# Optimization experiments

Measured on AMD Instinct MI355X. Metric: run time of the kernel, lower is better.

Reference implementation:

```python
import jax, jax.numpy as jnp
import numpy as np

TGT_LEN = 1024
MEM_LEN = 1024
SAME_LENGTH = True
D_MODEL = 2048
BATCH = 4


def _make_ft_real(tgt_len: int, mem_len: int, same_length: bool) -> jnp.ndarray:
    """Build the banded Fourier mixing matrix. Since the module's input x is real
    and only .real of the output is returned, Re(FT @ x) == Re(FT) @ x, so we
    precompute only the real part (this also matches the kernel-headroom note:
    the imaginary output is never used)."""
    qlen = tgt_len
    klen = tgt_len + mem_len
    flen = klen - qlen + 1
    m = np.outer(np.arange(qlen), np.arange(flen))
    ft = np.exp(2j * np.pi * m / flen) / np.sqrt(flen)  # [qlen, flen] complex
    ft = np.pad(ft, ((0, 0), (klen - flen, 0)))          # left-pad to [qlen, klen]
    for i in range(qlen):  # setup-time numpy loop over fixed qlen rows (not traced)
        ft[i] = np.roll(ft[i], -(qlen - i - 1))
    ft = np.tril(ft, klen - qlen)
    if same_length:
        ft = np.triu(ft, 0)
    return jnp.asarray(ft.real.astype(np.float32))


_FT_REAL = _make_ft_real(TGT_LEN, MEM_LEN, SAME_LENGTH)  # [tgt_len, tgt_len+mem_len]


def setup_inputs() -> dict:
    key = jax.random.key(0)
    k1, k2 = jax.random.split(key)
    klen = TGT_LEN + MEM_LEN
    x = jax.random.normal(k1, (BATCH, klen, D_MODEL), dtype=jnp.float32)
    p = jax.random.normal(k2, (BATCH, klen, D_MODEL), dtype=jnp.float32)
    return {"x": x, "p": p, "qlen": TGT_LEN, "add_position": 1}


def reference(x, p, qlen, add_position):
    # Dropout is identity in eval mode (deterministic reference).
    if add_position:
        x = x + p
    klen = x.shape[1]
    ft = _FT_REAL[-qlen:, -klen:]                    # [qlen, klen]
    scale = np.float32(1.0 / np.sqrt(klen))
    # Banded token-mixing matmul; real part only (x is real).
    out = jnp.einsum("lm,bmd->bld", ft, x) * scale   # [B, qlen, D]
    return out
```

## Files before the change

kernel.cpp:

```cpp
#include <hip/hip_runtime.h>
#include <hip/hip_bf16.h>
#include <cstdint>

#define QLEN   1024
#define KLEN   2048
#define DMODEL 2048
#define BATCH  4
#define FLEN   (KLEN - QLEN + 1)

typedef __bf16 bf16x8 __attribute__((ext_vector_type(8)));
typedef float  f32x4  __attribute__((ext_vector_type(4)));

__device__ __align__(16) __bf16 g_ft[(size_t)QLEN * KLEN];
__device__ __align__(16) __bf16 g_yt[(size_t)BATCH * DMODEL * KLEN];

typedef __attribute__((address_space(1))) void gvoid;
typedef __attribute__((address_space(3))) void svoid;

__device__ __forceinline__ void async_load16(const void* g, void* lds) {
  gvoid* gp = (gvoid*)(uintptr_t)g;
  svoid* sp = (svoid*)(uint32_t)(uintptr_t)lds;
  __builtin_amdgcn_global_load_lds(gp, sp, 16, 0, 0);
}

#define YT_UNITS (BATCH * (KLEN / 8) * (DMODEL / 64))
#define FT_UNITS ((QLEN * KLEN) / 512)

__global__ __launch_bounds__(256) void prep_kernel(const float* __restrict__ x,
                                                   const float* __restrict__ p,
                                                   const int* __restrict__ addp,
                                                   __bf16* __restrict__ ftp,
                                                   __bf16* __restrict__ ytp) {
  __bf16* ft = ftp ? ftp : g_ft;
  __bf16* yt = ytp ? ytp : g_yt;
  const int lane  = threadIdx.x & 63;
  const int gw    = (blockIdx.x * 256 + threadIdx.x) >> 6;
  const int nw    = gridDim.x * 4;
  const int doadd = *addp;

  for (int u = gw; u < YT_UNITS + FT_UNITS; u += nw) {
    if (u < YT_UNITS) {
      const int b  = u >> 13;
      const int r5 = u & 8191;
      const int mt = r5 >> 5;
      const int db = r5 & 31;
      const int d  = db * 64 + lane;
      const float* xp = x + ((size_t)b * KLEN + mt * 8) * DMODEL + d;
      float v[8];
#pragma unroll
      for (int i = 0; i < 8; ++i) v[i] = xp[(size_t)i * DMODEL];
      if (doadd) {
        const float* pp = p + ((size_t)b * KLEN + mt * 8) * DMODEL + d;
#pragma unroll
        for (int i = 0; i < 8; ++i) v[i] += pp[(size_t)i * DMODEL];
      }
      bf16x8 o;
#pragma unroll
      for (int i = 0; i < 8; ++i) o[i] = (__bf16)v[i];
      *(bf16x8*)(yt + ((size_t)b * (KLEN / 8) * DMODEL + (size_t)mt * DMODEL + d) * 8) = o;
    } else {
      const int uu = (u - YT_UNITS) * 64 + lane;
      const int l  = uu >> 8;
      const int m0 = (uu & 255) * 8;
      const int j0 = m0 - l;
      bf16x8 o = {};
      if (j0 + 7 >= 0 && j0 < FLEN) {
        const float w     = 6.283185307179586f / (float)FLEN;
        const float scale = 1.0f / sqrtf((float)FLEN * (float)KLEN);
#pragma unroll
        for (int i = 0; i < 8; ++i) {
          const int j = j0 + i;
          float vv = 0.0f;
          if (j >= 0 && j < FLEN) {
            const int rr = (l * j) % FLEN;
            vv = cosf((float)rr * w) * scale;
          }
          o[i] = (__bf16)vv;
        }
      }
      *(bf16x8*)(ft + (size_t)uu * 8) = o;
    }
  }
}

#define BM 128
#define BN 128
#define BK 64

__global__ __launch_bounds__(256) void gemm_kernel(float* __restrict__ out,
                                                   const __bf16* __restrict__ ftq,
                                                   const __bf16* __restrict__ ytq) {
  __shared__ __align__(16) __bf16 As[BM * BK];
  __shared__ __align__(16) __bf16 Bs[BN * BK];
  const int bn = blockIdx.x, bm = blockIdx.y, b = blockIdx.z;
  const int l0 = bm * BM, d0 = bn * BN;
  const int tid  = threadIdx.x;
  const int lane = tid & 63;
  const int wave = tid >> 6;
  const int wr = wave >> 1, wc = wave & 1;
  const int col = lane & 15, quad = lane >> 4;

  f32x4 acc[4][4] = {};

  const int t0 = l0 >> 6;
  const int t1 = (l0 + BM - 1 + FLEN - 1) >> 6;
  const __bf16* ftp = ftq ? ftq : g_ft;
  const __bf16* ytp = (ytq ? ytq : g_yt) + (size_t)b * DMODEL * KLEN;

  for (int t = t0; t <= t1; ++t) {
    const int k0 = t * BK;
#pragma unroll
    for (int s = 0; s < 4; ++s) {
      const int cb  = wave * 256 + s * 64;
      const int lc  = cb + lane;
      const int row = lc >> 3;
      const int gc8 = (lc & 7) ^ (row & 7);
      async_load16(ftp + (size_t)(l0 + row) * KLEN + k0 + gc8 * 8, As + cb * 8);
    }
#pragma unroll
    for (int s = 0; s < 4; ++s) {
      const int idx = wave * 256 + s * 64 + lane;
      const int c   = idx >> 7;
      const int dd  = idx & 127;
      async_load16(ytp + ((size_t)(t * 8 + c) * DMODEL + (d0 + dd)) * 8, Bs + (size_t)idx * 8);
    }
    __syncthreads();

#pragma unroll
    for (int kk = 0; kk < 2; ++kk) {
      bf16x8 af[4], bq[4];
      const int c8 = kk * 4 + quad;
#pragma unroll
      for (int ti = 0; ti < 4; ++ti) {
        const int r = wr * 64 + ti * 16 + col;
        af[ti] = *(const bf16x8*)(As + (size_t)((r << 3) + (c8 ^ (r & 7))) * 8);
      }
#pragma unroll
      for (int tj = 0; tj < 4; ++tj) {
        const int r = wc * 64 + tj * 16 + col;
        bq[tj] = *(const bf16x8*)(Bs + (size_t)((c8 << 7) + r) * 8);
      }
#pragma unroll
      for (int ti = 0; ti < 4; ++ti)
#pragma unroll
        for (int tj = 0; tj < 4; ++tj)
          acc[ti][tj] = __builtin_amdgcn_mfma_f32_16x16x32_bf16(af[ti], bq[tj], acc[ti][tj], 0, 0, 0);
    }
    __syncthreads();
  }

#pragma unroll
  for (int ti = 0; ti < 4; ++ti) {
    const int l = l0 + wr * 64 + ti * 16 + quad * 4;
#pragma unroll
    for (int tj = 0; tj < 4; ++tj) {
      const int d = d0 + wc * 64 + tj * 16 + col;
      float* op = out + (size_t)b * QLEN * DMODEL + (size_t)l * DMODEL + d;
#pragma unroll
      for (int r2 = 0; r2 < 4; ++r2) op[(size_t)r2 * DMODEL] = acc[ti][tj][r2];
    }
  }
}

extern "C" void kernel_launch(void* const* d_in, const int* in_sizes, int n_in,
                              void* d_out, int out_size, void* d_ws, size_t ws_size,
                              hipStream_t stream) {
  const float* x   = (const float*)d_in[0];
  const float* p   = (const float*)d_in[1];
  const int* addp  = (const int*)d_in[3];
  float* out = (float*)d_out;

  const size_t FT_BYTES = (size_t)QLEN * KLEN * sizeof(__bf16);
  const size_t YT_BYTES = (size_t)BATCH * DMODEL * KLEN * sizeof(__bf16);
  __bf16* ft = nullptr;
  __bf16* yt = nullptr;
  char* ws = (char*)d_ws;
  if (ws && ws_size >= FT_BYTES + YT_BYTES) {
    ft = (__bf16*)ws;
    yt = (__bf16*)(ws + FT_BYTES);
  } else if (ws && ws_size >= YT_BYTES) {
    yt = (__bf16*)ws;
  }

  prep_kernel<<<dim3(2048), dim3(256), 0, stream>>>(x, p, addp, ft, yt);
  gemm_kernel<<<dim3(DMODEL / BN, QLEN / BM, BATCH), dim3(256), 0, stream>>>(out, ft, yt);
}
```

Baseline: 188.7 us.

## Vectorize prep loads with float4 and permute yt layout to match

The prep kernel now reads x and p as 16-byte float4 vectors, four d-columns per lane, and issues all loads before converting. It writes the bf16 transposed buffer in a new permuted layout. The GEMM's B-tile address calculation is changed to match that layout, and the prep grid is halved. The goal is to cut the memory-bound prep cost from scalar 4-byte loads. The trade-offs are that p is now always loaded even when add_position is zero, and the GEMM B-tile reads are less contiguous.

Result: slower. 194.2 us (+2.9%).

```diff
diff --git a/kernel.cpp b/kernel.cpp
--- a/kernel.cpp
+++ b/kernel.cpp
@@ -23,8 +23,9 @@
   __builtin_amdgcn_global_load_lds(gp, sp, 16, 0, 0);
 }
 
-#define YT_UNITS (BATCH * (KLEN / 8) * (DMODEL / 64))
+#define YT_UNITS (BATCH * (KLEN / 8) * (DMODEL / 256))
 #define FT_UNITS ((QLEN * KLEN) / 512)
+#define PREP_BLOCKS 1024
 
 __global__ __launch_bounds__(256) void prep_kernel(const float* __restrict__ x,
                                                    const float* __restrict__ p,
@@ -36,28 +37,30 @@
   const int lane  = threadIdx.x & 63;
   const int gw    = (blockIdx.x * 256 + threadIdx.x) >> 6;
   const int nw    = gridDim.x * 4;
-  const int doadd = *addp;
+  const float addf = (*addp) ? 1.0f : 0.0f;
 
   for (int u = gw; u < YT_UNITS + FT_UNITS; u += nw) {
     if (u < YT_UNITS) {
-      const int b  = u >> 13;
-      const int r5 = u & 8191;
-      const int mt = r5 >> 5;
-      const int db = r5 & 31;
-      const int d  = db * 64 + lane;
-      const float* xp = x + ((size_t)b * KLEN + mt * 8) * DMODEL + d;
-      float v[8];
+      const int b  = u >> 11;
+      const int r  = u & 2047;
+      const int mt = r >> 3;
+      const int g  = r & 7;
+      const f32x4* xp4 = (const f32x4*)(x + ((size_t)b * KLEN + mt * 8) * DMODEL + g * 256 + 4 * lane);
+      const f32x4* pp4 = (const f32x4*)(p + ((size_t)b * KLEN + mt * 8) * DMODEL + g * 256 + 4 * lane);
+      f32x4 vx[8], vp[8];
 #pragma unroll
-      for (int i = 0; i < 8; ++i) v[i] = xp[(size_t)i * DMODEL];
-      if (doadd) {
-        const float* pp = p + ((size_t)b * KLEN + mt * 8) * DMODEL + d;
+      for (int i = 0; i < 8; ++i) vx[i] = xp4[(size_t)i * (DMODEL / 4)];
 #pragma unroll
-        for (int i = 0; i < 8; ++i) v[i] += pp[(size_t)i * DMODEL];
+      for (int i = 0; i < 8; ++i) vp[i] = pp4[(size_t)i * (DMODEL / 4)];
+      __builtin_amdgcn_sched_barrier(0);
+      __bf16* op = yt + (size_t)b * (size_t)(DMODEL * KLEN) + mt * 16384 + g * 2048 + lane * 8;
+#pragma unroll
+      for (int j = 0; j < 4; ++j) {
+        bf16x8 o;
+#pragma unroll
+        for (int i = 0; i < 8; ++i) o[i] = (__bf16)(vx[i][j] + addf * vp[i][j]);
+        *(bf16x8*)(op + j * 512) = o;
       }
-      bf16x8 o;
-#pragma unroll
-      for (int i = 0; i < 8; ++i) o[i] = (__bf16)v[i];
-      *(bf16x8*)(yt + ((size_t)b * (KLEN / 8) * DMODEL + (size_t)mt * DMODEL + d) * 8) = o;
     } else {
       const int uu = (u - YT_UNITS) * 64 + lane;
       const int l  = uu >> 8;
@@ -122,7 +125,10 @@
       const int idx = wave * 256 + s * 64 + lane;
       const int c   = idx >> 7;
       const int dd  = idx & 127;
-      async_load16(ytp + ((size_t)(t * 8 + c) * DMODEL + (d0 + dd)) * 8, Bs + (size_t)idx * 8);
+      const int mtg = t * 8 + c;
+      const size_t src = (size_t)mtg * 16384 + (bn >> 1) * 2048
+                       + (dd & 3) * 512 + (((bn & 1) << 5) + (dd >> 2)) * 8;
+      async_load16(ytp + src, Bs + (size_t)idx * 8);
     }
     __syncthreads();
 
@@ -182,6 +188,6 @@
     yt = (__bf16*)ws;
   }
 
-  prep_kernel<<<dim3(2048), dim3(256), 0, stream>>>(x, p, addp, ft, yt);
+  prep_kernel<<<dim3(PREP_BLOCKS), dim3(256), 0, stream>>>(x, p, addp, ft, yt);
   gemm_kernel<<<dim3(DMODEL / BN, QLEN / BM, BATCH), dim3(256), 0, stream>>>(out, ft, yt);
 }
```

## Fuse prep and GEMM into one kernel with per-batch flag dependencies

Applied to the files above, without the earlier changes.

Merges the conversion/FT-generation prep kernel and the banded GEMM into a single launch where prep blocks signal atomic counters and GEMM blocks spin-wait on the FT flag and their batch's flag. This lets GEMM work for early batches overlap with prep of later batches and removes the full inter-kernel barrier. It adds a tiny flag-reset kernel, spin-waits that depend on block dispatch order to avoid deadlock, and shares LDS allocation across all block roles.

New measurement: 389.2 us. 2.06x slower.

```diff
diff --git a/kernel.cpp b/kernel.cpp
--- a/kernel.cpp
+++ b/kernel.cpp
@@ -13,6 +13,7 @@
 
 __device__ __align__(16) __bf16 g_ft[(size_t)QLEN * KLEN];
 __device__ __align__(16) __bf16 g_yt[(size_t)BATCH * DMODEL * KLEN];
+__device__ int g_flags[8];
 
 typedef __attribute__((address_space(1))) void gvoid;
 typedef __attribute__((address_space(3))) void svoid;
@@ -23,50 +24,48 @@
   __builtin_amdgcn_global_load_lds(gp, sp, 16, 0, 0);
 }
 
-#define YT_UNITS (BATCH * (KLEN / 8) * (DMODEL / 64))
-#define FT_UNITS ((QLEN * KLEN) / 512)
-
-__global__ __launch_bounds__(256) void prep_kernel(const float* __restrict__ x,
-                                                   const float* __restrict__ p,
-                                                   const int* __restrict__ addp,
-                                                   __bf16* __restrict__ ftp,
-                                                   __bf16* __restrict__ ytp) {
+#define BM 128
+#define BN 128
+#define BK 64
+
+#define FT_BLOCKS  256
+#define YT_BLOCKS  (BATCH * 256)
+#define GEMM_PER_B 128
+#define GRID_TOTAL (FT_BLOCKS + YT_BLOCKS + BATCH * GEMM_PER_B)
+
+__global__ void init_flags_kernel(int* flagsp) {
+  int* flags = flagsp ? flagsp : g_flags;
+  if (threadIdx.x < 8) flags[threadIdx.x] = 0;
+}
+
+__global__ __launch_bounds__(256, 4) void fused_kernel(const float* __restrict__ x,
+                                                       const float* __restrict__ p,
+                                                       const int* __restrict__ addp,
+                                                       __bf16* __restrict__ ftp,
+                                                       __bf16* __restrict__ ytp,
+                                                       int* __restrict__ flagsp,
+                                                       float* __restrict__ out) {
+  __shared__ __align__(16) __bf16 As[BM * BK];
+  __shared__ __align__(16) __bf16 Bs[BN * BK];
   __bf16* ft = ftp ? ftp : g_ft;
   __bf16* yt = ytp ? ytp : g_yt;
-  const int lane  = threadIdx.x & 63;
-  const int gw    = (blockIdx.x * 256 + threadIdx.x) >> 6;
-  const int nw    = gridDim.x * 4;
-  const int doadd = *addp;
-
-  for (int u = gw; u < YT_UNITS + FT_UNITS; u += nw) {
-    if (u < YT_UNITS) {
-      const int b  = u >> 13;
-      const int r5 = u & 8191;
-      const int mt = r5 >> 5;
-      const int db = r5 & 31;
-      const int d  = db * 64 + lane;
-      const float* xp = x + ((size_t)b * KLEN + mt * 8) * DMODEL + d;
-      float v[8];
-#pragma unroll
-      for (int i = 0; i < 8; ++i) v[i] = xp[(size_t)i * DMODEL];
-      if (doadd) {
-        const float* pp = p + ((size_t)b * KLEN + mt * 8) * DMODEL + d;
-#pragma unroll
-        for (int i = 0; i < 8; ++i) v[i] += pp[(size_t)i * DMODEL];
-      }
-      bf16x8 o;
-#pragma unroll
-      for (int i = 0; i < 8; ++i) o[i] = (__bf16)v[i];
-      *(bf16x8*)(yt + ((size_t)b * (KLEN / 8) * DMODEL + (size_t)mt * DMODEL + d) * 8) = o;
-    } else {
-      const int uu = (u - YT_UNITS) * 64 + lane;
+  int* flags = flagsp ? flagsp : g_flags;
+  const int tid  = threadIdx.x;
+  const int lane = tid & 63;
+  const int wave = tid >> 6;
+  const int bid  = blockIdx.x;
+
+  if (bid < FT_BLOCKS) {
+    const float w     = 6.283185307179586f / (float)FLEN;
+    const float scale = 1.0f / sqrtf((float)FLEN * (float)KLEN);
+#pragma unroll
+    for (int s = 0; s < 4; ++s) {
+      const int uu = bid * 1024 + s * 256 + tid;
       const int l  = uu >> 8;
       const int m0 = (uu & 255) * 8;
       const int j0 = m0 - l;
       bf16x8 o = {};
       if (j0 + 7 >= 0 && j0 < FLEN) {
-        const float w     = 6.283185307179586f / (float)FLEN;
-        const float scale = 1.0f / sqrtf((float)FLEN * (float)KLEN);
 #pragma unroll
         for (int i = 0; i < 8; ++i) {
           const int j = j0 + i;
@@ -80,32 +79,66 @@
       }
       *(bf16x8*)(ft + (size_t)uu * 8) = o;
     }
-  }
-}
-
-#define BM 128
-#define BN 128
-#define BK 64
-
-__global__ __launch_bounds__(256) void gemm_kernel(float* __restrict__ out,
-                                                   const __bf16* __restrict__ ftq,
-                                                   const __bf16* __restrict__ ytq) {
-  __shared__ __align__(16) __bf16 As[BM * BK];
-  __shared__ __align__(16) __bf16 Bs[BN * BK];
-  const int bn = blockIdx.x, bm = blockIdx.y, b = blockIdx.z;
+    __syncthreads();
+    if (tid == 0) {
+      __threadfence();
+      __hip_atomic_fetch_add(&flags[4], 1, __ATOMIC_RELEASE, __HIP_MEMORY_SCOPE_AGENT);
+    }
+    return;
+  }
+
+  if (bid < FT_BLOCKS + YT_BLOCKS) {
+    const int idx = bid - FT_BLOCKS;
+    const int b = idx >> 8, mt = idx & 255;
+    const int doadd = *addp;
+    __bf16* outp = yt + ((size_t)b * 256 + mt) * (size_t)(DMODEL * 8);
+#pragma unroll
+    for (int q = 0; q < 8; ++q) {
+      const int d = (wave * 8 + q) * 64 + lane;
+      const float* xp = x + ((size_t)b * KLEN + mt * 8) * DMODEL + d;
+      float v[8];
+#pragma unroll
+      for (int i = 0; i < 8; ++i) v[i] = xp[(size_t)i * DMODEL];
+      if (doadd) {
+        const float* pp = p + ((size_t)b * KLEN + mt * 8) * DMODEL + d;
+#pragma unroll
+        for (int i = 0; i < 8; ++i) v[i] += pp[(size_t)i * DMODEL];
+      }
+      bf16x8 o;
+#pragma unroll
+      for (int i = 0; i < 8; ++i) o[i] = (__bf16)v[i];
+      *(bf16x8*)(outp + (size_t)d * 8) = o;
+    }
+    __syncthreads();
+    if (tid == 0) {
+      __threadfence();
+      __hip_atomic_fetch_add(&flags[b], 1, __ATOMIC_RELEASE, __HIP_MEMORY_SCOPE_AGENT);
+    }
+    return;
+  }
+
+  const int gidx = bid - FT_BLOCKS - YT_BLOCKS;
+  const int b = gidx >> 7;
+  const int inner = gidx & 127;
+  const int bm = inner >> 4, bn = inner & 15;
+  if (tid == 0) {
+    while (__hip_atomic_load(&flags[4], __ATOMIC_ACQUIRE, __HIP_MEMORY_SCOPE_AGENT) < FT_BLOCKS)
+      __builtin_amdgcn_s_sleep(8);
+    while (__hip_atomic_load(&flags[b], __ATOMIC_ACQUIRE, __HIP_MEMORY_SCOPE_AGENT) < 256)
+      __builtin_amdgcn_s_sleep(8);
+  }
+  __syncthreads();
+  __threadfence();
+
   const int l0 = bm * BM, d0 = bn * BN;
-  const int tid  = threadIdx.x;
-  const int lane = tid & 63;
-  const int wave = tid >> 6;
   const int wr = wave >> 1, wc = wave & 1;
   const int col = lane & 15, quad = lane >> 4;
-
   f32x4 acc[4][4] = {};
 
   const int t0 = l0 >> 6;
   const int t1 = (l0 + BM - 1 + FLEN - 1) >> 6;
-  const __bf16* ftp = ftq ? ftq : g_ft;
-  const __bf16* ytp = (ytq ? ytq : g_yt) + (size_t)b * DMODEL * KLEN;
+  const __bf16* ftb = ft;
+  const __bf16* ytb = yt + (size_t)b * DMODEL * KLEN;
 
   for (int t = t0; t <= t1; ++t) {
     const int k0 = t * BK;
@@ -115,14 +148,14 @@
       const int lc  = cb + lane;
       const int row = lc >> 3;
       const int gc8 = (lc & 7) ^ (row & 7);
-      async_load16(ftp + (size_t)(l0 + row) * KLEN + k0 + gc8 * 8, As + cb * 8);
+      async_load16(ftb + (size_t)(l0 + row) * KLEN + k0 + gc8 * 8, As + cb * 8);
     }
 #pragma unroll
     for (int s = 0; s < 4; ++s) {
       const int idx = wave * 256 + s * 64 + lane;
       const int c   = idx >> 7;
       const int dd  = idx & 127;
-      async_load16(ytp + ((size_t)(t * 8 + c) * DMODEL + (d0 + dd)) * 8, Bs + (size_t)idx * 8);
+      async_load16(ytb + ((size_t)(t * 8 + c) * DMODEL + (d0 + dd)) * 8, Bs + (size_t)idx * 8);
     }
     __syncthreads();
 
@@ -174,14 +207,19 @@
   const size_t YT_BYTES = (size_t)BATCH * DMODEL * KLEN * sizeof(__bf16);
   __bf16* ft = nullptr;
   __bf16* yt = nullptr;
+  int* flags = nullptr;
   char* ws = (char*)d_ws;
-  if (ws && ws_size >= FT_BYTES + YT_BYTES) {
+  if (ws && ws_size >= FT_BYTES + YT_BYTES + 256) {
+    ft = (__bf16*)ws;
+    yt = (__bf16*)(ws + FT_BYTES);
+    flags = (int*)(ws + FT_BYTES + YT_BYTES);
+  } else if (ws && ws_size >= FT_BYTES + YT_BYTES) {
     ft = (__bf16*)ws;
     yt = (__bf16*)(ws + FT_BYTES);
   } else if (ws && ws_size >= YT_BYTES) {
     yt = (__bf16*)ws;
   }
 
-  prep_kernel<<<dim3(2048), dim3(256), 0, stream>>>(x, p, addp, ft, yt);
-  gemm_kernel<<<dim3(DMODEL / BN, QLEN / BM, BATCH), dim3(256), 0, stream>>>(out, ft, yt);
-}
+  init_flags_kernel<<<dim3(1), dim3(64), 0, stream>>>(flags);
+  fused_kernel<<<dim3(GRID_TOTAL), dim3(256), 0, stream>>>(x, p, addp, ft, yt, flags, out);
+}
```
